# Kernel tuning notes

Hardware: AMD Instinct MI355X
Metric: run time of the kernel (lower is better)

## Reference

```python
import jax, jax.numpy as jnp
import numpy as np

EPS = 1e-5

def _gcn_norm(edge_index, num_nodes):
    # add self loops (improved=False -> fill value 1.0), symmetric normalization
    src = jnp.concatenate([edge_index[0], jnp.arange(num_nodes)])
    dst = jnp.concatenate([edge_index[1], jnp.arange(num_nodes)])
    w = jnp.ones(src.shape[0], dtype=jnp.float32)
    deg = jax.ops.segment_sum(w, dst, num_segments=num_nodes)
    dinv = jnp.where(deg > 0, 1.0 / jnp.sqrt(deg), 0.0)
    norm = dinv[src] * dinv[dst]  # [E+N]
    return src, dst, norm

def _gcn_conv(x, W, src, dst, norm, num_nodes):
    h = x @ W                      # [N, out]
    msg = h[src] * norm[:, None]   # gather + scale, [E+N, out]
    return jax.ops.segment_sum(msg, dst, num_segments=num_nodes)

def _bn_relu(x, gamma, beta):
    # BatchNorm1d in training mode: biased batch stats over the node dim
    m = x.mean(axis=0)
    v = x.var(axis=0)
    return jax.nn.relu((x - m) * jax.lax.rsqrt(v + EPS) * gamma + beta)

def setup_inputs() -> dict:
    key = jax.random.key(0)
    ks = jax.random.split(key, 12)
    N, E, D_IN, H, D_OUT, DEPTH = 100000, 1600000, 3, 128, 1, 9
    x = jax.random.normal(ks[0], (N, D_IN), dtype=jnp.float32)
    edge_index = jax.random.randint(ks[1], (2, E), 0, N, dtype=jnp.int64)
    s = 1.0 / np.sqrt(H)
    W0 = jax.random.normal(ks[2], (D_IN, H), jnp.float32) / np.sqrt(D_IN)
    Ws1 = jax.random.normal(ks[3], (DEPTH, H, H), jnp.float32) * s
    g1 = jnp.ones((DEPTH + 1, H), jnp.float32)
    b1 = jnp.zeros((DEPTH + 1, H), jnp.float32)
    Ws2 = jax.random.normal(ks[4], (DEPTH - 1, H, H), jnp.float32) * s
    g2 = jnp.ones((DEPTH - 1, H), jnp.float32)
    b2 = jnp.zeros((DEPTH - 1, H), jnp.float32)
    Wout = jax.random.normal(ks[5], (H, D_OUT), jnp.float32) * s
    return {"x": x, "edge_index": edge_index, "W0": W0, "Ws1": Ws1, "g1": g1,
            "b1": b1, "Ws2": Ws2, "g2": g2, "b2": b2, "Wout": Wout}

def reference(x, edge_index, W0, Ws1, g1, b1, Ws2, g2, b2, Wout):
    N = x.shape[0]
    depth = Ws1.shape[0]  # 9
    src, dst, norm = _gcn_norm(edge_index, N)
    # conv1[0]
    h = _bn_relu(_gcn_conv(x, W0, src, dst, norm, N), g1[0], b1[0])
    xs = [h]
    for i in range(1, depth + 1):
        h = _bn_relu(_gcn_conv(h, Ws1[i - 1], src, dst, norm, N), g1[i], b1[i])
        if i < depth:
            xs.append(h)
    for i in range(depth):
        j = depth - i - 1
        h = h + xs[j]
        if i < depth - 1:
            h = _bn_relu(_gcn_conv(h, Ws2[i], src, dst, norm, N), g2[i], b2[i])
        else:
            h = jax.nn.sigmoid(_gcn_conv(h, Wout, src, dst, norm, N))
    return h
```

## Files before the change

kernel.cpp:

```cpp
#include <hip/hip_runtime.h>
#include <hip/hip_bf16.h>

#define EPSV 1e-5f
#define NSTRIPE 16

typedef unsigned int uint;
typedef unsigned short ushort;
typedef __attribute__((ext_vector_type(8))) __bf16 bf16x8;
typedef __attribute__((ext_vector_type(4))) float f32x4;

static __device__ __forceinline__ float bf2f(ushort u) {
    return __uint_as_float(((uint)u) << 16);
}
static __device__ __forceinline__ ushort f2bf(float f) {
    __hip_bfloat16 h = __float2bfloat16(f);
    return __builtin_bit_cast(ushort, h);
}


static __device__ __forceinline__ float e4m3_dec(unsigned char b) {
    int s = b >> 7, E = (b >> 3) & 15, m = b & 7;
    float v = (E == 0) ? (float)m * 0.001953125f
                       : (float)(8 + m) * 0.125f * exp2f((float)(E - 7));
    return s ? -v : v;
}
static __device__ __forceinline__ unsigned char e4m3_enc(float f) {
    unsigned su = (__float_as_uint(f) >> 24) & 0x80u;
    float a = fabsf(f);
    if (!(a < 448.f)) return (unsigned char)(su | 0x7E);
    if (a < 0.015625f) {
        int m = (int)rintf(a * 512.f);
        return (unsigned char)(su | (m >= 8 ? 0x08 : m));
    }
    int e;
    frexpf(a, &e);
    int E = e - 1 + 7;
    float mant = a * exp2f((float)(1 - e)) - 1.0f;
    int mi = (int)rintf(mant * 8.f);
    if (mi >= 8) { mi = 0; E++; }
    if (E >= 16) return (unsigned char)(su | 0x7E);
    if (E == 15 && mi == 7) mi = 6;
    return (unsigned char)(su | (E << 3) | mi);
}


template <typename T> struct IOV;
template <> struct IOV<float> {
    static __device__ __forceinline__ float2 ld2(const float* p) { return *(const float2*)p; }
    static __device__ __forceinline__ void st2(float* p, float a, float b) {
        *(float2*)p = make_float2(a, b);
    }
    static __device__ __forceinline__ void ld8(const float* p, float* v) {
        float4 a = ((const float4*)p)[0], b = ((const float4*)p)[1];
        v[0] = a.x; v[1] = a.y; v[2] = a.z; v[3] = a.w;
        v[4] = b.x; v[5] = b.y; v[6] = b.z; v[7] = b.w;
    }
    static __device__ __forceinline__ void st8(float* p, const float* v) {
        ((float4*)p)[0] = make_float4(v[0], v[1], v[2], v[3]);
        ((float4*)p)[1] = make_float4(v[4], v[5], v[6], v[7]);
    }
};
template <> struct IOV<ushort> {
    static __device__ __forceinline__ float2 ld2(const ushort* p) {
        uint u = *(const uint*)p;
        return make_float2(bf2f((ushort)u), bf2f((ushort)(u >> 16)));
    }
    static __device__ __forceinline__ void st2(ushort* p, float a, float b) {
        *(uint*)p = (uint)f2bf(a) | ((uint)f2bf(b) << 16);
    }
    static __device__ __forceinline__ void ld8(const ushort* p, float* v) {
        uint4 u = *(const uint4*)p;
        v[0] = bf2f((ushort)u.x); v[1] = bf2f((ushort)(u.x >> 16));
        v[2] = bf2f((ushort)u.y); v[3] = bf2f((ushort)(u.y >> 16));
        v[4] = bf2f((ushort)u.z); v[5] = bf2f((ushort)(u.z >> 16));
        v[6] = bf2f((ushort)u.w); v[7] = bf2f((ushort)(u.w >> 16));
    }
    static __device__ __forceinline__ void st8(ushort* p, const float* v) {
        uint4 u;
        u.x = (uint)f2bf(v[0]) | ((uint)f2bf(v[1]) << 16);
        u.y = (uint)f2bf(v[2]) | ((uint)f2bf(v[3]) << 16);
        u.z = (uint)f2bf(v[4]) | ((uint)f2bf(v[5]) << 16);
        u.w = (uint)f2bf(v[6]) | ((uint)f2bf(v[7]) << 16);
        *(uint4*)p = u;
    }
};
template <> struct IOV<unsigned char> {
    static __device__ __forceinline__ float2 ld2(const unsigned char* p) {
        ushort u = *(const ushort*)p;
        return make_float2(e4m3_dec((unsigned char)u), e4m3_dec((unsigned char)(u >> 8)));
    }
    static __device__ __forceinline__ void st2(unsigned char* p, float a, float b) {
        *(ushort*)p = (ushort)e4m3_enc(a) | ((ushort)e4m3_enc(b) << 8);
    }
    static __device__ __forceinline__ void ld8(const unsigned char* p, float* v) {
        uint2 u = *(const uint2*)p;
#pragma unroll
        for (int j = 0; j < 4; j++) v[j] = e4m3_dec((unsigned char)(u.x >> (8 * j)));
#pragma unroll
        for (int j = 0; j < 4; j++) v[4 + j] = e4m3_dec((unsigned char)(u.y >> (8 * j)));
    }
    static __device__ __forceinline__ void st8(unsigned char* p, const float* v) {
        uint2 u = {0, 0};
#pragma unroll
        for (int j = 0; j < 4; j++) u.x |= (uint)e4m3_enc(v[j]) << (8 * j);
#pragma unroll
        for (int j = 0; j < 4; j++) u.y |= (uint)e4m3_enc(v[4 + j]) << (8 * j);
        *(uint2*)p = u;
    }
};


__global__ void k_count(const int* __restrict__ dst, int* __restrict__ cnt, int E) {
    int e = blockIdx.x * blockDim.x + threadIdx.x;
    if (e < E) atomicAdd(&cnt[dst[e]], 1);
}

__global__ void k_scan1(const int* __restrict__ cnt, int* __restrict__ bsum, int N) {
    __shared__ int s[256];
    int i = blockIdx.x * 256 + threadIdx.x;
    s[threadIdx.x] = (i < N) ? ((cnt[i] + 15) & ~15) : 0;
    __syncthreads();
    for (int o = 128; o > 0; o >>= 1) {
        if (threadIdx.x < o) s[threadIdx.x] += s[threadIdx.x + o];
        __syncthreads();
    }
    if (threadIdx.x == 0) bsum[blockIdx.x] = s[0];
}

__global__ void k_scan2(int* __restrict__ bsum, int B) {
    __shared__ int s[1024];
    int t = threadIdx.x;
    int orig = (t < B) ? bsum[t] : 0;
    s[t] = orig;
    __syncthreads();
    for (int o = 1; o < 1024; o <<= 1) {
        int v = (t >= o) ? s[t - o] : 0;
        __syncthreads();
        s[t] += v;
        __syncthreads();
    }
    if (t < B) bsum[t] = s[t] - orig;
}

__global__ void k_scan3(const int* __restrict__ cnt, const int* __restrict__ bsum,
                        int* __restrict__ roff, int* __restrict__ cursor,
                        float* __restrict__ dinv, int N) {
    __shared__ int s[256];
    int i = blockIdx.x * 256 + threadIdx.x;
    int v = (i < N) ? cnt[i] : 0;
    int pv = (v + 15) & ~15;
    s[threadIdx.x] = pv;
    __syncthreads();
    for (int o = 1; o < 256; o <<= 1) {
        int u = (threadIdx.x >= o) ? s[threadIdx.x - o] : 0;
        __syncthreads();
        s[threadIdx.x] += u;
        __syncthreads();
    }
    if (i < N) {
        int off = bsum[blockIdx.x] + s[threadIdx.x] - pv;
        roff[i] = off;
        cursor[i] = off;
        dinv[i] = rsqrtf((float)(v + 1));
        if (i == N - 1) roff[N] = off + pv;
    }
}

__global__ void k_scatter(const int* __restrict__ src, const int* __restrict__ dst,
                          const float* __restrict__ dinv, int* __restrict__ cursor,
                          int2* __restrict__ ev, int E) {
    int e = blockIdx.x * blockDim.x + threadIdx.x;
    if (e < E) {
        int s = src[e], d = dst[e];
        int p = atomicAdd(&cursor[d], 1);
        int2 pk;
        pk.x = s;
        pk.y = __float_as_int(dinv[s] * dinv[d]);
        ev[p] = pk;
    }
}

__global__ void k_pad(const int* __restrict__ cursor, const int* __restrict__ roff,
                      int2* __restrict__ ev, int N) {
    int i = blockIdx.x * blockDim.x + threadIdx.x;
    if (i >= N) return;
    int p = cursor[i], e = roff[i + 1];
    int2 pk;
    pk.x = i;
    pk.y = 0;
    for (; p < e; p++) ev[p] = pk;
}

__global__ void k_prepw(const float* __restrict__ Ws1, const float* __restrict__ Ws2,
                        ushort* __restrict__ whi, ushort* __restrict__ wlo) {
    int idx = blockIdx.x * blockDim.x + threadIdx.x;
    if (idx >= 17 * 16384) return;
    int L = idx >> 14, r = idx & 16383;
    int f = r >> 9, e = r & 511, lane = e >> 3, j = e & 7;
    int n = (f >> 2) * 16 + (lane & 15);
    int k = (f & 3) * 32 + (lane >> 4) * 8 + j;
    const float* W = (L < 9) ? (Ws1 + (size_t)L * 16384) : (Ws2 + (size_t)(L - 9) * 16384);
    float w = W[(size_t)k * 128 + n];
    ushort hi = f2bf(w);
    whi[idx] = hi;
    wlo[idx] = f2bf(w - bf2f(hi));
}


__global__ void k_spmm3(const float* __restrict__ X, const int2* __restrict__ ev,
                        const int* __restrict__ roff, const float* __restrict__ dinv,
                        float* __restrict__ XA, int N) {
    int i = blockIdx.x * blockDim.x + threadIdx.x;
    if (i >= N) return;
    float di = dinv[i];
    float w0 = di * di;
    float a0 = X[(size_t)i * 3 + 0] * w0;
    float a1 = X[(size_t)i * 3 + 1] * w0;
    float a2 = X[(size_t)i * 3 + 2] * w0;
    int je = roff[i + 1];
    for (int j = roff[i]; j < je; j++) {
        int2 e = ev[j];
        float w = __int_as_float(e.y);
        a0 += X[(size_t)e.x * 3 + 0] * w;
        a1 += X[(size_t)e.x * 3 + 1] * w;
        a2 += X[(size_t)e.x * 3 + 2] * w;
    }
    XA[(size_t)i * 3 + 0] = a0;
    XA[(size_t)i * 3 + 1] = a1;
    XA[(size_t)i * 3 + 2] = a2;
}

template <typename ZT>
__global__ __launch_bounds__(256) void k_spmm_stats(
    const ushort* __restrict__ H, const int2* __restrict__ ev,
    const int* __restrict__ roff, const float* __restrict__ dinv,
    ZT* __restrict__ Y, float* __restrict__ st, int N) {
    int lane = threadIdx.x & 63, wv = threadIdx.x >> 6;
    const uint* Hu = (const uint*)H;
    float s0 = 0.f, s1 = 0.f, q0 = 0.f, q1 = 0.f;

#pragma unroll
    for (int r = 0; r < 4; r++) {
        int i = blockIdx.x * 16 + wv * 4 + r;
        if (i >= N) break;
        float di = dinv[i];
        float ws = di * di;
        uint u = Hu[(size_t)i * 64 + lane];
        float a0 = bf2f((ushort)u) * ws, a1 = bf2f((ushort)(u >> 16)) * ws;
        int j = roff[i], je = roff[i + 1];
        for (; j < je; j += 16) {
            int2 e[16];
            uint uu[16];
#pragma unroll
            for (int t = 0; t < 16; t++) e[t] = ev[j + t];
#pragma unroll
            for (int t = 0; t < 16; t++) uu[t] = Hu[(size_t)e[t].x * 64 + lane];
#pragma unroll
            for (int t = 0; t < 16; t++) {
                float w = __int_as_float(e[t].y);
                a0 += bf2f((ushort)uu[t]) * w;
                a1 += bf2f((ushort)(uu[t] >> 16)) * w;
            }
        }
        IOV<ZT>::st2(&Y[(size_t)i * 128 + 2 * lane], a0, a1);
        s0 += a0; q0 += a0 * a0;
        s1 += a1; q1 += a1 * a1;
    }

    __shared__ float ls[4][64][4];
    ls[wv][lane][0] = s0; ls[wv][lane][1] = s1;
    ls[wv][lane][2] = q0; ls[wv][lane][3] = q1;
    __syncthreads();
    if (wv == 0) {
        s0 = ls[0][lane][0] + ls[1][lane][0] + ls[2][lane][0] + ls[3][lane][0];
        s1 = ls[0][lane][1] + ls[1][lane][1] + ls[2][lane][1] + ls[3][lane][1];
        q0 = ls[0][lane][2] + ls[1][lane][2] + ls[2][lane][2] + ls[3][lane][2];
        q1 = ls[0][lane][3] + ls[1][lane][3] + ls[2][lane][3] + ls[3][lane][3];
        float* stp = st + (size_t)(blockIdx.x & (NSTRIPE - 1)) * 256;
        atomicAdd(&stp[2 * lane], s0);
        atomicAdd(&stp[2 * lane + 1], s1);
        atomicAdd(&stp[128 + 2 * lane], q0);
        atomicAdd(&stp[129 + 2 * lane], q1);
    }
}

__global__ void k_spmm1(const float* __restrict__ T, const int2* __restrict__ ev,
                        const int* __restrict__ roff, const float* __restrict__ dinv,
                        float* __restrict__ out, int N) {
    int i = blockIdx.x * blockDim.x + threadIdx.x;
    if (i >= N) return;
    float di = dinv[i];
    float a = T[i] * di * di;
    int je = roff[i + 1];
    for (int j = roff[i]; j < je; j++) {
        int2 e = ev[j];
        a += T[e.x] * __int_as_float(e.y);
    }
    out[i] = 1.0f / (1.0f + expf(-a));
}

__global__ void k_bnfin(const float* __restrict__ st, const float* __restrict__ g,
                        const float* __restrict__ b, float* __restrict__ aff, float invN) {
    int c = threadIdx.x;
    float S = 0.f, Q = 0.f;
    for (int s = 0; s < NSTRIPE; s++) {
        S += st[(size_t)s * 256 + c];
        Q += st[(size_t)s * 256 + 128 + c];
    }
    float m = S * invN;
    float var = Q * invN - m * m;
    float sc = g[c] * rsqrtf(var + EPSV);
    aff[c] = sc;
    aff[128 + c] = b[c] - m * sc;
}


template <typename ZT>
__global__ __launch_bounds__(256) void k_gemm3_stats(
    const float* __restrict__ XA, const float* __restrict__ W0,
    ZT* __restrict__ Y, float* __restrict__ st, int N) {
    int lane = threadIdx.x & 63, wv = threadIdx.x >> 6;
    int i = blockIdx.x * 4 + wv;
    float y0 = 0.f, y1 = 0.f;
    if (i < N) {
        int c0 = lane * 2;
        float x0 = XA[(size_t)i * 3], x1 = XA[(size_t)i * 3 + 1], x2 = XA[(size_t)i * 3 + 2];
        y0 = x0 * W0[c0] + x1 * W0[128 + c0] + x2 * W0[256 + c0];
        y1 = x0 * W0[c0 + 1] + x1 * W0[128 + c0 + 1] + x2 * W0[256 + c0 + 1];
        IOV<ZT>::st2(&Y[(size_t)i * 128 + c0], y0, y1);
    }
    __shared__ float ls[4][64][4];
    ls[wv][lane][0] = y0; ls[wv][lane][1] = y1;
    ls[wv][lane][2] = y0 * y0; ls[wv][lane][3] = y1 * y1;
    __syncthreads();
    if (wv == 0) {
        float s0 = ls[0][lane][0] + ls[1][lane][0] + ls[2][lane][0] + ls[3][lane][0];
        float s1 = ls[0][lane][1] + ls[1][lane][1] + ls[2][lane][1] + ls[3][lane][1];
        float q0 = ls[0][lane][2] + ls[1][lane][2] + ls[2][lane][2] + ls[3][lane][2];
        float q1 = ls[0][lane][3] + ls[1][lane][3] + ls[2][lane][3] + ls[3][lane][3];
        float* stp = st + (size_t)(blockIdx.x & (NSTRIPE - 1)) * 256;
        atomicAdd(&stp[2 * lane], s0);
        atomicAdd(&stp[2 * lane + 1], s1);
        atomicAdd(&stp[128 + 2 * lane], q0);
        atomicAdd(&stp[129 + 2 * lane], q1);
    }
}

template <typename ZT, typename SKT>
__global__ __launch_bounds__(256) void k_gemm_mfma(
    const ZT* __restrict__ Z, const SKT* __restrict__ skip_in, SKT* __restrict__ skip_out,
    const float* __restrict__ st, const float* __restrict__ gz, const float* __restrict__ bz,
    const ushort* __restrict__ whi, const ushort* __restrict__ wlo,
    ushort* __restrict__ H, float invN, int N) {
    __shared__ ushort sW[16384];
    __shared__ float sA[256];
    int tid = threadIdx.x;
    int wave = tid >> 6, lane = tid & 63;
    int l15 = lane & 15, quad = lane >> 4;

    {
        float acc = 0.f;
#pragma unroll
        for (int s = 0; s < NSTRIPE; s++) acc += st[(size_t)s * 256 + tid];
        sA[tid] = acc;
    }
    {
        const uint4* src = (const uint4*)whi;
#pragma unroll
        for (int t = 0; t < 8; t++) ((uint4*)sW)[tid + 256 * t] = src[tid + 256 * t];
    }
    __syncthreads();
    if (tid < 128) {
        float S = sA[tid], Q = sA[128 + tid];
        float m = S * invN;
        float var = Q * invN - m * m;
        float sc = gz[tid] * rsqrtf(var + EPSV);
        sA[tid] = sc;
        sA[128 + tid] = bz[tid] - m * sc;
    }
    __syncthreads();

    int row = blockIdx.x * 64 + wave * 16 + l15;
    size_t rowc = (size_t)(row < N ? row : N - 1);

    bf16x8 ahi[4];
#pragma unroll
    for (int kc = 0; kc < 4; kc++) {
        int c0 = kc * 32 + quad * 8;
        float v[8];
        IOV<ZT>::ld8(&Z[rowc * 128 + c0], v);
        float av[8];
#pragma unroll
        for (int jj = 0; jj < 8; jj++) {
            float t = v[jj] * sA[c0 + jj] + sA[128 + c0 + jj];
            av[jj] = fmaxf(t, 0.f);
        }
        if (skip_out && row < N) IOV<SKT>::st8(&skip_out[rowc * 128 + c0], av);
        if (skip_in) {
            float w2[8];
            IOV<SKT>::ld8(&skip_in[rowc * 128 + c0], w2);
#pragma unroll
            for (int jj = 0; jj < 8; jj++) av[jj] += w2[jj];
        }
        bf16x8 fh;
#pragma unroll
        for (int jj = 0; jj < 8; jj++) fh[jj] = (__bf16)av[jj];
        ahi[kc] = fh;
    }

    f32x4 acc[8];
#pragma unroll
    for (int ct = 0; ct < 8; ct++) {
        f32x4 z0 = {0.f, 0.f, 0.f, 0.f};
        acc[ct] = z0;
    }

#pragma unroll
    for (int ct = 0; ct < 8; ct++) {
#pragma unroll
        for (int kc = 0; kc < 4; kc++) {
            bf16x8 b = *(const bf16x8*)&sW[(ct * 4 + kc) * 512 + lane * 8];
            acc[ct] = __builtin_amdgcn_mfma_f32_16x16x32_bf16(ahi[kc], b, acc[ct], 0, 0, 0);
        }
    }
    __syncthreads();
    {
        const uint4* src = (const uint4*)wlo;
#pragma unroll
        for (int t = 0; t < 8; t++) ((uint4*)sW)[tid + 256 * t] = src[tid + 256 * t];
    }
    __syncthreads();
#pragma unroll
    for (int ct = 0; ct < 8; ct++) {
#pragma unroll
        for (int kc = 0; kc < 4; kc++) {
            bf16x8 b = *(const bf16x8*)&sW[(ct * 4 + kc) * 512 + lane * 8];
            acc[ct] = __builtin_amdgcn_mfma_f32_16x16x32_bf16(ahi[kc], b, acc[ct], 0, 0, 0);
        }
    }
    __syncthreads();
    ushort* sC = sW;
#pragma unroll
    for (int ct = 0; ct < 8; ct++)
#pragma unroll
        for (int reg = 0; reg < 4; reg++) {
            int r = wave * 16 + quad * 4 + reg;
            sC[r * 136 + ct * 16 + l15] = f2bf(acc[ct][reg]);
        }
    __syncthreads();
    for (int t = tid; t < 1024; t += 256) {
        int r = t >> 4, c4 = t & 15;
        int grow = blockIdx.x * 64 + r;
        if (grow < N)
            ((uint4*)(H + (size_t)grow * 128))[c4] = *(const uint4*)&sC[r * 136 + c4 * 8];
    }
}

template <typename ZT, typename SKT>
__global__ __launch_bounds__(256) void k_dot(
    const ZT* __restrict__ Z, const SKT* __restrict__ S0,
    const float* __restrict__ aff, const float* __restrict__ Wout,
    float* __restrict__ T, int N) {
    int i = blockIdx.x * 4 + (threadIdx.x >> 6);
    if (i >= N) return;
    int lane = threadIdx.x & 63;
    int c0 = 2 * lane, c1 = c0 + 1;
    float2 z = IOV<ZT>::ld2(&Z[(size_t)i * 128 + c0]);
    float2 s = IOV<SKT>::ld2(&S0[(size_t)i * 128 + c0]);
    float p0 = fmaxf(z.x * aff[c0] + aff[128 + c0], 0.f) + s.x;
    float p1 = fmaxf(z.y * aff[c1] + aff[128 + c1], 0.f) + s.y;
    float a = p0 * Wout[c0] + p1 * Wout[c1];
    for (int o = 32; o > 0; o >>= 1) a += __shfl_down(a, o);
    if (lane == 0) T[i] = a;
}


template <typename ZT, typename SKT>
static void run_all(const float* x, const int* src, const int* dst, const float* W0,
                    const float* Ws1, const float* g1, const float* b1,
                    const float* Ws2, const float* g2, const float* b2,
                    const float* Wout, float* out, char* ws, int N, int E,
                    hipStream_t stream) {
    char* p = ws;
    auto alloc = [&](size_t bytes) -> void* {
        void* r = (void*)p;
        p += (bytes + 255) & ~(size_t)255;
        return r;
    };
    size_t Epad = (size_t)E + 15 * (size_t)N + 16;
    int*   roff   = (int*)alloc((size_t)(N + 1) * 4);
    float* dinv   = (float*)alloc((size_t)N * 4);
    int2*  ev     = (int2*)alloc(Epad * 8);
    int*   bsum   = (int*)alloc(4096);
    float* st_all = (float*)alloc((size_t)18 * NSTRIPE * 256 * 4);
    float* aff    = (float*)alloc(1024);
    ushort* whi   = (ushort*)alloc((size_t)17 * 16384 * 2);
    ushort* wlo   = (ushort*)alloc((size_t)17 * 16384 * 2);
    size_t nz = (size_t)N * 128;
    ushort* hb = (ushort*)alloc(nz * 2);
    ZT* zb = (ZT*)alloc(nz * sizeof(ZT));
    SKT* skips = (SKT*)alloc((size_t)9 * nz * sizeof(SKT));
    auto skip = [&](int s) { return skips + (size_t)s * nz; };
    auto stg  = [&](int s) { return st_all + (size_t)s * NSTRIPE * 256; };

    int* cnt    = (int*)skip(8);
    int* cursor = (int*)((char*)skip(8) + (((size_t)N * 4 + 255) & ~(size_t)255));
    float* xa   = (float*)hb;
    float* tbuf = (float*)hb;

    float invN = 1.0f / (float)N;
    auto gb = [&](int stage, const float** g, const float** b) {
        if (stage <= 9) { *g = g1 + (size_t)stage * 128; *b = b1 + (size_t)stage * 128; }
        else { *g = g2 + (size_t)(stage - 10) * 128; *b = b2 + (size_t)(stage - 10) * 128; }
    };

    hipMemsetAsync(st_all, 0, (size_t)18 * NSTRIPE * 256 * 4, stream);
    hipMemsetAsync(cnt, 0, (size_t)N * 4, stream);
    k_count<<<(E + 255) / 256, 256, 0, stream>>>(dst, cnt, E);
    int B = (N + 255) / 256;
    k_scan1<<<B, 256, 0, stream>>>(cnt, bsum, N);
    k_scan2<<<1, 1024, 0, stream>>>(bsum, B);
    k_scan3<<<B, 256, 0, stream>>>(cnt, bsum, roff, cursor, dinv, N);
    k_scatter<<<(E + 255) / 256, 256, 0, stream>>>(src, dst, dinv, cursor, ev, E);
    k_pad<<<(N + 255) / 256, 256, 0, stream>>>(cursor, roff, ev, N);
    k_prepw<<<(17 * 16384 + 255) / 256, 256, 0, stream>>>(Ws1, Ws2, whi, wlo);

    int gg = (N + 63) / 64;
    int gs4 = (N + 3) / 4;
    int gs16 = (N + 15) / 16;

    k_spmm3<<<(N + 255) / 256, 256, 0, stream>>>(x, ev, roff, dinv, xa, N);
    k_gemm3_stats<ZT><<<gs4, 256, 0, stream>>>(xa, W0, zb, stg(0), N);

    for (int l = 1; l <= 9; l++) {
        const float *gzp, *bzp;
        gb(l - 1, &gzp, &bzp);
        k_gemm_mfma<ZT, SKT><<<gg, 256, 0, stream>>>(
            zb, (const SKT*)nullptr, skip(l - 1), stg(l - 1), gzp, bzp,
            whi + (size_t)(l - 1) * 16384, wlo + (size_t)(l - 1) * 16384, hb, invN, N);
        k_spmm_stats<ZT><<<gs16, 256, 0, stream>>>(hb, ev, roff, dinv, zb, stg(l), N);
    }

    for (int i = 0; i < 8; i++) {
        int zs = 9 + i;
        const float *gzp, *bzp;
        gb(zs, &gzp, &bzp);
        k_gemm_mfma<ZT, SKT><<<gg, 256, 0, stream>>>(
            zb, skip(8 - i), (SKT*)nullptr, stg(zs), gzp, bzp,
            whi + (size_t)(9 + i) * 16384, wlo + (size_t)(9 + i) * 16384, hb, invN, N);
        k_spmm_stats<ZT><<<gs16, 256, 0, stream>>>(hb, ev, roff, dinv, zb, stg(10 + i), N);
    }

    const float *gzp, *bzp;
    gb(17, &gzp, &bzp);
    k_bnfin<<<1, 128, 0, stream>>>(stg(17), gzp, bzp, aff, invN);
    k_dot<ZT, SKT><<<gs4, 256, 0, stream>>>(zb, skip(0), aff, Wout, tbuf, N);
    k_spmm1<<<(N + 255) / 256, 256, 0, stream>>>(tbuf, ev, roff, dinv, out, N);
}


extern "C" void kernel_launch(void* const* d_in, const int* in_sizes, int n_in,
                              void* d_out, int out_size, void* d_ws, size_t ws_size,
                              hipStream_t stream) {
    const float* x    = (const float*)d_in[0];
    const int*   ei   = (const int*)d_in[1];
    const float* W0   = (const float*)d_in[2];
    const float* Ws1  = (const float*)d_in[3];
    const float* g1   = (const float*)d_in[4];
    const float* b1   = (const float*)d_in[5];
    const float* Ws2  = (const float*)d_in[6];
    const float* g2   = (const float*)d_in[7];
    const float* b2   = (const float*)d_in[8];
    const float* Wout = (const float*)d_in[9];
    float* out = (float*)d_out;

    int N = in_sizes[0] / 3;
    int E = in_sizes[1] / 2;
    const int* src = ei;
    const int* dst = ei + E;

    size_t nz = (size_t)N * 128;
    size_t Epad = (size_t)E + 15 * (size_t)N + 16;
    auto need = [&](size_t zbytes, size_t skbytes) -> size_t {
        size_t t = 0;
        auto add = [&](size_t b) { t += (b + 255) & ~(size_t)255; };
        add((size_t)(N + 1) * 4);
        add((size_t)N * 4);
        add(Epad * 8);
        add(4096);
        add((size_t)18 * NSTRIPE * 256 * 4);
        add(1024);
        add((size_t)17 * 16384 * 2);
        add((size_t)17 * 16384 * 2);
        add(nz * 2);
        add(nz * zbytes);
        add((size_t)9 * nz * skbytes);
        return t;
    };

    char* ws = (char*)d_ws;
    if (need(4, 2) <= ws_size)
        run_all<float, ushort>(x, src, dst, W0, Ws1, g1, b1, Ws2, g2, b2, Wout, out, ws, N, E, stream);
    else if (need(4, 1) <= ws_size)
        run_all<float, unsigned char>(x, src, dst, W0, Ws1, g1, b1, Ws2, g2, b2, Wout, out, ws, N, E, stream);
    else
        run_all<ushort, unsigned char>(x, src, dst, W0, Ws1, g1, b1, Ws2, g2, b2, Wout, out, ws, N, E, stream);
}
```

Baseline: 2.130 ms.

## Split SpMM feature columns across two blocks and batch rows in first GEMM

```diff
diff --git a/kernel.cpp b/kernel.cpp
--- a/kernel.cpp
+++ b/kernel.cpp
@@ -50,6 +50,7 @@
     static __device__ __forceinline__ void st2(float* p, float a, float b) {
         *(float2*)p = make_float2(a, b);
     }
+    static __device__ __forceinline__ void st1(float* p, float v) { *p = v; }
     static __device__ __forceinline__ void ld8(const float* p, float* v) {
         float4 a = ((const float4*)p)[0], b = ((const float4*)p)[1];
         v[0] = a.x; v[1] = a.y; v[2] = a.z; v[3] = a.w;
@@ -68,6 +69,7 @@
     static __device__ __forceinline__ void st2(ushort* p, float a, float b) {
         *(uint*)p = (uint)f2bf(a) | ((uint)f2bf(b) << 16);
     }
+    static __device__ __forceinline__ void st1(ushort* p, float v) { *p = f2bf(v); }
     static __device__ __forceinline__ void ld8(const ushort* p, float* v) {
         uint4 u = *(const uint4*)p;
         v[0] = bf2f((ushort)u.x); v[1] = bf2f((ushort)(u.x >> 16));
@@ -92,6 +94,7 @@
     static __device__ __forceinline__ void st2(unsigned char* p, float a, float b) {
         *(ushort*)p = (ushort)e4m3_enc(a) | ((ushort)e4m3_enc(b) << 8);
     }
+    static __device__ __forceinline__ void st1(unsigned char* p, float v) { *p = e4m3_enc(v); }
     static __device__ __forceinline__ void ld8(const unsigned char* p, float* v) {
         uint2 u = *(const uint2*)p;
 #pragma unroll
@@ -236,51 +239,43 @@
     const int* __restrict__ roff, const float* __restrict__ dinv,
     ZT* __restrict__ Y, float* __restrict__ st, int N) {
     int lane = threadIdx.x & 63, wv = threadIdx.x >> 6;
-    const uint* Hu = (const uint*)H;
-    float s0 = 0.f, s1 = 0.f, q0 = 0.f, q1 = 0.f;
+    int half = blockIdx.x & 1;
+    int rblk = blockIdx.x >> 1;
+    int c = half * 64 + lane;
+    float s = 0.f, q = 0.f;
 
 #pragma unroll
     for (int r = 0; r < 4; r++) {
-        int i = blockIdx.x * 16 + wv * 4 + r;
+        int i = rblk * 16 + wv * 4 + r;
         if (i >= N) break;
         float di = dinv[i];
-        float ws = di * di;
-        uint u = Hu[(size_t)i * 64 + lane];
-        float a0 = bf2f((ushort)u) * ws, a1 = bf2f((ushort)(u >> 16)) * ws;
+        float a = bf2f(H[(size_t)i * 128 + c]) * di * di;
         int j = roff[i], je = roff[i + 1];
         for (; j < je; j += 16) {
             int2 e[16];
-            uint uu[16];
+            ushort hv[16];
 #pragma unroll
             for (int t = 0; t < 16; t++) e[t] = ev[j + t];
 #pragma unroll
-            for (int t = 0; t < 16; t++) uu[t] = Hu[(size_t)e[t].x * 64 + lane];
-#pragma unroll
-            for (int t = 0; t < 16; t++) {
-                float w = __int_as_float(e[t].y);
-                a0 += bf2f((ushort)uu[t]) * w;
-                a1 += bf2f((ushort)(uu[t] >> 16)) * w;
-            }
+            for (int t = 0; t < 16; t++) hv[t] = H[(size_t)e[t].x * 128 + c];
+#pragma unroll
+            for (int t = 0; t < 16; t++) a += bf2f(hv[t]) * __int_as_float(e[t].y);
         }
-        IOV<ZT>::st2(&Y[(size_t)i * 128 + 2 * lane], a0, a1);
-        s0 += a0; q0 += a0 * a0;
-        s1 += a1; q1 += a1 * a1;
-    }
-
-    __shared__ float ls[4][64][4];
-    ls[wv][lane][0] = s0; ls[wv][lane][1] = s1;
-    ls[wv][lane][2] = q0; ls[wv][lane][3] = q1;
+        IOV<ZT>::st1(&Y[(size_t)i * 128 + c], a);
+        s += a;
+        q += a * a;
+    }
+
+    __shared__ float ls[4][64][2];
+    ls[wv][lane][0] = s;
+    ls[wv][lane][1] = q;
     __syncthreads();
     if (wv == 0) {
-        s0 = ls[0][lane][0] + ls[1][lane][0] + ls[2][lane][0] + ls[3][lane][0];
-        s1 = ls[0][lane][1] + ls[1][lane][1] + ls[2][lane][1] + ls[3][lane][1];
-        q0 = ls[0][lane][2] + ls[1][lane][2] + ls[2][lane][2] + ls[3][lane][2];
-        q1 = ls[0][lane][3] + ls[1][lane][3] + ls[2][lane][3] + ls[3][lane][3];
-        float* stp = st + (size_t)(blockIdx.x & (NSTRIPE - 1)) * 256;
-        atomicAdd(&stp[2 * lane], s0);
-        atomicAdd(&stp[2 * lane + 1], s1);
-        atomicAdd(&stp[128 + 2 * lane], q0);
-        atomicAdd(&stp[129 + 2 * lane], q1);
+        s = ls[0][lane][0] + ls[1][lane][0] + ls[2][lane][0] + ls[3][lane][0];
+        q = ls[0][lane][1] + ls[1][lane][1] + ls[2][lane][1] + ls[3][lane][1];
+        float* stp = st + (size_t)(rblk & (NSTRIPE - 1)) * 256;
+        atomicAdd(&stp[c], s);
+        atomicAdd(&stp[128 + c], q);
     }
 }
 
@@ -320,24 +315,30 @@
     const float* __restrict__ XA, const float* __restrict__ W0,
     ZT* __restrict__ Y, float* __restrict__ st, int N) {
     int lane = threadIdx.x & 63, wv = threadIdx.x >> 6;
-    int i = blockIdx.x * 4 + wv;
-    float y0 = 0.f, y1 = 0.f;
-    if (i < N) {
-        int c0 = lane * 2;
+    int c0 = lane * 2;
+    float w00 = W0[c0], w10 = W0[128 + c0], w20 = W0[256 + c0];
+    float w01 = W0[c0 + 1], w11 = W0[128 + c0 + 1], w21 = W0[256 + c0 + 1];
+    float s0 = 0.f, s1 = 0.f, q0 = 0.f, q1 = 0.f;
+#pragma unroll
+    for (int r = 0; r < 4; r++) {
+        int i = blockIdx.x * 16 + wv * 4 + r;
+        if (i >= N) break;
         float x0 = XA[(size_t)i * 3], x1 = XA[(size_t)i * 3 + 1], x2 = XA[(size_t)i * 3 + 2];
-        y0 = x0 * W0[c0] + x1 * W0[128 + c0] + x2 * W0[256 + c0];
-        y1 = x0 * W0[c0 + 1] + x1 * W0[128 + c0 + 1] + x2 * W0[256 + c0 + 1];
+        float y0 = x0 * w00 + x1 * w10 + x2 * w20;
+        float y1 = x0 * w01 + x1 * w11 + x2 * w21;
         IOV<ZT>::st2(&Y[(size_t)i * 128 + c0], y0, y1);
+        s0 += y0; q0 += y0 * y0;
+        s1 += y1; q1 += y1 * y1;
     }
     __shared__ float ls[4][64][4];
-    ls[wv][lane][0] = y0; ls[wv][lane][1] = y1;
-    ls[wv][lane][2] = y0 * y0; ls[wv][lane][3] = y1 * y1;
+    ls[wv][lane][0] = s0; ls[wv][lane][1] = s1;
+    ls[wv][lane][2] = q0; ls[wv][lane][3] = q1;
     __syncthreads();
     if (wv == 0) {
-        float s0 = ls[0][lane][0] + ls[1][lane][0] + ls[2][lane][0] + ls[3][lane][0];
-        float s1 = ls[0][lane][1] + ls[1][lane][1] + ls[2][lane][1] + ls[3][lane][1];
-        float q0 = ls[0][lane][2] + ls[1][lane][2] + ls[2][lane][2] + ls[3][lane][2];
-        float q1 = ls[0][lane][3] + ls[1][lane][3] + ls[2][lane][3] + ls[3][lane][3];
+        s0 = ls[0][lane][0] + ls[1][lane][0] + ls[2][lane][0] + ls[3][lane][0];
+        s1 = ls[0][lane][1] + ls[1][lane][1] + ls[2][lane][1] + ls[3][lane][1];
+        q0 = ls[0][lane][2] + ls[1][lane][2] + ls[2][lane][2] + ls[3][lane][2];
+        q1 = ls[0][lane][3] + ls[1][lane][3] + ls[2][lane][3] + ls[3][lane][3];
         float* stp = st + (size_t)(blockIdx.x & (NSTRIPE - 1)) * 256;
         atomicAdd(&stp[2 * lane], s0);
         atomicAdd(&stp[2 * lane + 1], s1);
@@ -528,9 +529,10 @@
     int gg = (N + 63) / 64;
     int gs4 = (N + 3) / 4;
     int gs16 = (N + 15) / 16;
+    int gh = 2 * gs16;
 
     k_spmm3<<<(N + 255) / 256, 256, 0, stream>>>(x, ev, roff, dinv, xa, N);
-    k_gemm3_stats<ZT><<<gs4, 256, 0, stream>>>(xa, W0, zb, stg(0), N);
+    k_gemm3_stats<ZT><<<gs16, 256, 0, stream>>>(xa, W0, zb, stg(0), N);
 
     for (int l = 1; l <= 9; l++) {
         const float *gzp, *bzp;
@@ -538,7 +540,7 @@
         k_gemm_mfma<ZT, SKT><<<gg, 256, 0, stream>>>(
             zb, (const SKT*)nullptr, skip(l - 1), stg(l - 1), gzp, bzp,
             whi + (size_t)(l - 1) * 16384, wlo + (size_t)(l - 1) * 16384, hb, invN, N);
-        k_spmm_stats<ZT><<<gs16, 256, 0, stream>>>(hb, ev, roff, dinv, zb, stg(l), N);
+        k_spmm_stats<ZT><<<gh, 256, 0, stream>>>(hb, ev, roff, dinv, zb, stg(l), N);
     }
 
     for (int i = 0; i < 8; i++) {
@@ -548,7 +550,7 @@
         k_gemm_mfma<ZT, SKT><<<gg, 256, 0, stream>>>(
             zb, skip(8 - i), (SKT*)nullptr, stg(zs), gzp, bzp,
             whi + (size_t)(9 + i) * 16384, wlo + (size_t)(9 + i) * 16384, hb, invN, N);
-        k_spmm_stats<ZT><<<gs16, 256, 0, stream>>>(hb, ev, roff, dinv, zb, stg(10 + i), N);
+        k_spmm_stats<ZT><<<gh, 256, 0, stream>>>(hb, ev, roff, dinv, zb, stg(10 + i), N);
     }
 
     const float *gzp, *bzp;
```

Result: slower. 2.645 ms (+24.2%).
